# Kernel tuning notes

Measured on AMD Instinct MI355X. Metric: run time of the kernel, lower is better.

The kernel has to match this reference:

```python
import jax, jax.numpy as jnp
import numpy as np

N_FEAT = 1024
N_LAYER = 4  # n_layer + 1 in the original module


def setup_inputs() -> dict:
    key = jax.random.key(0)
    kx, kw, kb = jax.random.split(key, 3)
    x = jax.random.normal(kx, (16384, N_FEAT), dtype=jnp.float32)
    weight_w = jax.random.normal(kw, (N_LAYER, N_FEAT), dtype=jnp.float32)
    weight_b = jax.random.normal(kb, (N_LAYER, N_FEAT), dtype=jnp.float32)
    return {"x": x, "weight_w": weight_w, "weight_b": weight_b}


def reference(x, weight_w, weight_b):
    # Original per layer: x_{i+1} = x0 @ x_i^T @ w_i + b_i + x_i  (per sample).
    # (x0 x_i^T) w = x0 * <x_i, w>, so we use the O(n) equivalent form and
    # never materialize the [B, n, n] outer product.
    x0 = x  # [B, n]
    xi = x0
    for i in range(N_LAYER):
        xiw = jnp.einsum("bn,n->b", xi, weight_w[i])  # [B]
        xi = x0 * xiw[:, None] + weight_b[i][None, :] + xi
    return xi
```

## Files before the change

kernel.cpp:

```cpp
#include <hip/hip_runtime.h>

#define N_FEAT 1024
#define N_LAYER 4
#define R 2

__global__ __launch_bounds__(256, 4) void crossnet_kernel(
    const float* __restrict__ x,
    const float* __restrict__ weight_w,
    const float* __restrict__ weight_b,
    float* __restrict__ out,
    int n_rows) {
  const int wave = threadIdx.x >> 6;
  const int lane = threadIdx.x & 63;
  const int row0 = (blockIdx.x * 4 + wave) * R;
  if (row0 >= n_rows) return;

  const float4* xq = (const float4*)x;
  float4* oq = (float4*)out;

  float4 x0[R * 4];
#pragma unroll
  for (int r = 0; r < R; ++r)
#pragma unroll
    for (int c = 0; c < 4; ++c)
      x0[r * 4 + c] = xq[(size_t)(row0 + r) * 256 + c * 64 + lane];

  float p[R * N_LAYER];
#pragma unroll
  for (int k = 0; k < R * N_LAYER; ++k) p[k] = 0.f;
  float e[N_LAYER] = {0.f, 0.f, 0.f, 0.f};

#pragma unroll
  for (int c = 0; c < 4; ++c) {
    float4 w[N_LAYER];
#pragma unroll
    for (int i = 0; i < N_LAYER; ++i)
      w[i] = ((const float4*)(weight_w + i * N_FEAT))[c * 64 + lane];

    float4 cum = make_float4(0.f, 0.f, 0.f, 0.f);
#pragma unroll
    for (int i = 0; i < N_LAYER; ++i) {
      if (i > 0)
        e[i] += cum.x * w[i].x + cum.y * w[i].y + cum.z * w[i].z + cum.w * w[i].w;
      float4 b = ((const float4*)(weight_b + i * N_FEAT))[c * 64 + lane];
      cum.x += b.x; cum.y += b.y; cum.z += b.z; cum.w += b.w;
    }

#pragma unroll
    for (int r = 0; r < R; ++r) {
      const float4 xv = x0[r * 4 + c];
#pragma unroll
      for (int i = 0; i < N_LAYER; ++i) {
        p[r * N_LAYER + i] += xv.x * w[i].x + xv.y * w[i].y +
                              xv.z * w[i].z + xv.w * w[i].w;
      }
    }
  }

#pragma unroll
  for (int off = 32; off > 0; off >>= 1) {
#pragma unroll
    for (int k = 0; k < R * N_LAYER; ++k) p[k] += __shfl_xor(p[k], off, 64);
#pragma unroll
    for (int i = 1; i < N_LAYER; ++i) e[i] += __shfl_xor(e[i], off, 64);
  }

  float A[R];
#pragma unroll
  for (int r = 0; r < R; ++r) {
    A[r] = 1.f;
#pragma unroll
    for (int i = 0; i < N_LAYER; ++i)
      A[r] += A[r] * p[r * N_LAYER + i] + e[i];
  }

#pragma unroll
  for (int c = 0; c < 4; ++c) {
    float4 cum = make_float4(0.f, 0.f, 0.f, 0.f);
#pragma unroll
    for (int i = 0; i < N_LAYER; ++i) {
      float4 b = ((const float4*)(weight_b + i * N_FEAT))[c * 64 + lane];
      cum.x += b.x; cum.y += b.y; cum.z += b.z; cum.w += b.w;
    }
#pragma unroll
    for (int r = 0; r < R; ++r) {
      const float4 xv = x0[r * 4 + c];
      float4 o;
      o.x = fmaf(xv.x, A[r], cum.x);
      o.y = fmaf(xv.y, A[r], cum.y);
      o.z = fmaf(xv.z, A[r], cum.z);
      o.w = fmaf(xv.w, A[r], cum.w);
      oq[(size_t)(row0 + r) * 256 + c * 64 + lane] = o;
    }
  }
}

extern "C" void kernel_launch(void* const* d_in, const int* in_sizes, int n_in,
                              void* d_out, int out_size, void* d_ws, size_t ws_size,
                              hipStream_t stream) {
  const float* x = (const float*)d_in[0];
  const float* ww = (const float*)d_in[1];
  const float* wb = (const float*)d_in[2];
  float* out = (float*)d_out;

  int n_rows = in_sizes[0] / N_FEAT;
  int rows_per_block = 4 * R;
  int n_blocks = (n_rows + rows_per_block - 1) / rows_per_block;
  crossnet_kernel<<<n_blocks, 256, 0, stream>>>(x, ww, wb, out, n_rows);
}
```

Before: 136.3 us.

## Split row columns across wave pairs and combine partial dots via shared memory

Each block now handles 16 rows with two waves per 8-row group, each wave covering half the columns; partial dot products are exchanged through shared memory after a block barrier. x is reloaded in the output phase instead of being held in registers, and bias cumulative sums are kept from the first pass. This aims to cut register pressure and raise loads in flight, at the cost of a __syncthreads and a second read of x that relies on cache hits.

```diff
diff --git a/kernel.cpp b/kernel.cpp
--- a/kernel.cpp
+++ b/kernel.cpp
@@ -2,7 +2,7 @@
 
 #define N_FEAT 1024
 #define N_LAYER 4
-#define R 2
+#define R 8
 
 __global__ __launch_bounds__(256, 4) void crossnet_kernel(
     const float* __restrict__ x,
@@ -12,47 +12,50 @@
     int n_rows) {
   const int wave = threadIdx.x >> 6;
   const int lane = threadIdx.x & 63;
-  const int row0 = (blockIdx.x * 4 + wave) * R;
+  const int rowgrp = wave >> 1;
+  const int half = wave & 1;
+  const int row0 = blockIdx.x * (2 * R) + rowgrp * R;
   if (row0 >= n_rows) return;
 
   const float4* xq = (const float4*)x;
   float4* oq = (float4*)out;
 
-  float4 x0[R * 4];
-#pragma unroll
-  for (int r = 0; r < R; ++r)
-#pragma unroll
-    for (int c = 0; c < 4; ++c)
-      x0[r * 4 + c] = xq[(size_t)(row0 + r) * 256 + c * 64 + lane];
-
   float p[R * N_LAYER];
 #pragma unroll
   for (int k = 0; k < R * N_LAYER; ++k) p[k] = 0.f;
   float e[N_LAYER] = {0.f, 0.f, 0.f, 0.f};
+  float4 csum[2];
 
 #pragma unroll
-  for (int c = 0; c < 4; ++c) {
+  for (int lc = 0; lc < 2; ++lc) {
+    const int col = (half * 2 + lc) * 64 + lane;
+
+    float4 xv[R];
+#pragma unroll
+    for (int r = 0; r < R; ++r)
+      xv[r] = xq[(size_t)(row0 + r) * 256 + col];
+
     float4 w[N_LAYER];
 #pragma unroll
     for (int i = 0; i < N_LAYER; ++i)
-      w[i] = ((const float4*)(weight_w + i * N_FEAT))[c * 64 + lane];
+      w[i] = ((const float4*)(weight_w + i * N_FEAT))[col];
 
     float4 cum = make_float4(0.f, 0.f, 0.f, 0.f);
 #pragma unroll
     for (int i = 0; i < N_LAYER; ++i) {
       if (i > 0)
         e[i] += cum.x * w[i].x + cum.y * w[i].y + cum.z * w[i].z + cum.w * w[i].w;
-      float4 b = ((const float4*)(weight_b + i * N_FEAT))[c * 64 + lane];
+      const float4 b = ((const float4*)(weight_b + i * N_FEAT))[col];
       cum.x += b.x; cum.y += b.y; cum.z += b.z; cum.w += b.w;
     }
+    csum[lc] = cum;
 
 #pragma unroll
     for (int r = 0; r < R; ++r) {
-      const float4 xv = x0[r * 4 + c];
 #pragma unroll
       for (int i = 0; i < N_LAYER; ++i) {
-        p[r * N_LAYER + i] += xv.x * w[i].x + xv.y * w[i].y +
-                              xv.z * w[i].z + xv.w * w[i].w;
+        p[r * N_LAYER + i] += xv[r].x * w[i].x + xv[r].y * w[i].y +
+                              xv[r].z * w[i].z + xv[r].w * w[i].w;
       }
     }
   }
@@ -65,32 +68,49 @@
     for (int i = 1; i < N_LAYER; ++i) e[i] += __shfl_xor(e[i], off, 64);
   }
 
+  __shared__ float pe[4][36];
+  if (lane == 0) {
+#pragma unroll
+    for (int k = 0; k < R * N_LAYER; ++k) pe[wave][k] = p[k];
+#pragma unroll
+    for (int i = 1; i < N_LAYER; ++i) pe[wave][32 + i] = e[i];
+  }
+  __syncthreads();
+  const int partner = wave ^ 1;
+  float pp[R * N_LAYER], ep[N_LAYER];
+#pragma unroll
+  for (int k = 0; k < R * N_LAYER; ++k) pp[k] = pe[partner][k];
+  ep[0] = 0.f;
+#pragma unroll
+  for (int i = 1; i < N_LAYER; ++i) ep[i] = pe[partner][32 + i];
+
   float A[R];
 #pragma unroll
   for (int r = 0; r < R; ++r) {
     A[r] = 1.f;
 #pragma unroll
-    for (int i = 0; i < N_LAYER; ++i)
-      A[r] += A[r] * p[r * N_LAYER + i] + e[i];
+    for (int i = 0; i < N_LAYER; ++i) {
+      const float pt = p[r * N_LAYER + i] + pp[r * N_LAYER + i];
+      const float et = e[i] + ep[i];
+      A[r] += A[r] * pt + et;
+    }
   }
 
 #pragma unroll
-  for (int c = 0; c < 4; ++c) {
-    float4 cum = make_float4(0.f, 0.f, 0.f, 0.f);
+  for (int lc = 0; lc < 2; ++lc) {
+    const int col = (half * 2 + lc) * 64 + lane;
+    float4 xv[R];
 #pragma unroll
-    for (int i = 0; i < N_LAYER; ++i) {
-      float4 b = ((const float4*)(weight_b + i * N_FEAT))[c * 64 + lane];
-      cum.x += b.x; cum.y += b.y; cum.z += b.z; cum.w += b.w;
-    }
+    for (int r = 0; r < R; ++r)
+      xv[r] = xq[(size_t)(row0 + r) * 256 + col];
 #pragma unroll
     for (int r = 0; r < R; ++r) {
-      const float4 xv = x0[r * 4 + c];
       float4 o;
-      o.x = fmaf(xv.x, A[r], cum.x);
-      o.y = fmaf(xv.y, A[r], cum.y);
-      o.z = fmaf(xv.z, A[r], cum.z);
-      o.w = fmaf(xv.w, A[r], cum.w);
-      oq[(size_t)(row0 + r) * 256 + c * 64 + lane] = o;
+      o.x = fmaf(xv[r].x, A[r], csum[lc].x);
+      o.y = fmaf(xv[r].y, A[r], csum[lc].y);
+      o.z = fmaf(xv[r].z, A[r], csum[lc].z);
+      o.w = fmaf(xv[r].w, A[r], csum[lc].w);
+      oq[(size_t)(row0 + r) * 256 + col] = o;
     }
   }
 }
@@ -103,8 +123,8 @@
   const float* wb = (const float*)d_in[2];
   float* out = (float*)d_out;
 
-  int n_rows = in_sizes[0] / N_FEAT;
-  int rows_per_block = 4 * R;
-  int n_blocks = (n_rows + rows_per_block - 1) / rows_per_block;
+  const int n_rows = in_sizes[0] / N_FEAT;
+  const int rows_per_block = 2 * R;
+  const int n_blocks = (n_rows + rows_per_block - 1) / rows_per_block;
   crossnet_kernel<<<n_blocks, 256, 0, stream>>>(x, ww, wb, out, n_rows);
 }
```

Result: faster. 128.6 us (-5.6%).

## Process four rows per wave with next-pair prefetch and LDS-staged weights

Applied to the files above, without the earlier changes.

Each wave now handles four rows as two pairs. The next pair's x is loaded while the current pair's dot products and outputs are computed. Weight vectors and the cumulative bias sum are staged once per wave in shared memory, and the layer-constant e terms are reduced once, so the global weight and bias reloads per row pair go away. This halves the block count and amortizes per-wave setup. In exchange, register pressure rises from holding two pairs of rows, which could lower occupancy.

```diff
diff --git a/kernel.cpp b/kernel.cpp
--- a/kernel.cpp
+++ b/kernel.cpp
@@ -2,7 +2,8 @@
 
 #define N_FEAT 1024
 #define N_LAYER 4
-#define R 2
+#define ROWS_PER_WAVE 4
+#define PAIR 2
 
 __global__ __launch_bounds__(256, 4) void crossnet_kernel(
     const float* __restrict__ x,
@@ -12,85 +13,110 @@
     int n_rows) {
   const int wave = threadIdx.x >> 6;
   const int lane = threadIdx.x & 63;
-  const int row0 = (blockIdx.x * 4 + wave) * R;
-  if (row0 >= n_rows) return;
+
+  __shared__ float4 w_lds[N_LAYER * 256];
+  __shared__ float4 csum_lds[256];
+
+  float e[N_LAYER] = {0.f, 0.f, 0.f, 0.f};
+#pragma unroll
+  for (int c = 0; c < 4; ++c) {
+    const int col = c * 64 + lane;
+    float4 wv[N_LAYER];
+#pragma unroll
+    for (int i = 0; i < N_LAYER; ++i) {
+      wv[i] = ((const float4*)(weight_w + i * N_FEAT))[col];
+      w_lds[i * 256 + col] = wv[i];
+    }
+    float4 cum = make_float4(0.f, 0.f, 0.f, 0.f);
+#pragma unroll
+    for (int i = 0; i < N_LAYER; ++i) {
+      if (i > 0)
+        e[i] += cum.x * wv[i].x + cum.y * wv[i].y +
+                cum.z * wv[i].z + cum.w * wv[i].w;
+      const float4 b = ((const float4*)(weight_b + i * N_FEAT))[col];
+      cum.x += b.x; cum.y += b.y; cum.z += b.z; cum.w += b.w;
+    }
+    csum_lds[col] = cum;
+  }
+#pragma unroll
+  for (int off = 32; off > 0; off >>= 1)
+#pragma unroll
+    for (int i = 1; i < N_LAYER; ++i) e[i] += __shfl_xor(e[i], off, 64);
+
+  const int g = blockIdx.x * 4 + wave;
+  const int row_base = g * ROWS_PER_WAVE;
+  if (row_base >= n_rows) return;
 
   const float4* xq = (const float4*)x;
   float4* oq = (float4*)out;
 
-  float4 x0[R * 4];
+  float4 xv[PAIR][4];
 #pragma unroll
-  for (int r = 0; r < R; ++r)
+  for (int r = 0; r < PAIR; ++r)
 #pragma unroll
     for (int c = 0; c < 4; ++c)
-      x0[r * 4 + c] = xq[(size_t)(row0 + r) * 256 + c * 64 + lane];
-
-  float p[R * N_LAYER];
-#pragma unroll
-  for (int k = 0; k < R * N_LAYER; ++k) p[k] = 0.f;
-  float e[N_LAYER] = {0.f, 0.f, 0.f, 0.f};
+      xv[r][c] = xq[(size_t)(row_base + r) * 256 + c * 64 + lane];
 
 #pragma unroll
-  for (int c = 0; c < 4; ++c) {
-    float4 w[N_LAYER];
+  for (int t = 0; t < ROWS_PER_WAVE / PAIR; ++t) {
+    const int pr = row_base + t * PAIR;
+
+    float4 nxt[PAIR][4];
+    if (t + 1 < ROWS_PER_WAVE / PAIR) {
 #pragma unroll
-    for (int i = 0; i < N_LAYER; ++i)
-      w[i] = ((const float4*)(weight_w + i * N_FEAT))[c * 64 + lane];
+      for (int r = 0; r < PAIR; ++r)
+#pragma unroll
+        for (int c = 0; c < 4; ++c)
+          nxt[r][c] = xq[(size_t)(pr + PAIR + r) * 256 + c * 64 + lane];
+    }
 
-    float4 cum = make_float4(0.f, 0.f, 0.f, 0.f);
+    float p[PAIR * N_LAYER];
 #pragma unroll
-    for (int i = 0; i < N_LAYER; ++i) {
-      if (i > 0)
-        e[i] += cum.x * w[i].x + cum.y * w[i].y + cum.z * w[i].z + cum.w * w[i].w;
-      float4 b = ((const float4*)(weight_b + i * N_FEAT))[c * 64 + lane];
-      cum.x += b.x; cum.y += b.y; cum.z += b.z; cum.w += b.w;
+    for (int k = 0; k < PAIR * N_LAYER; ++k) p[k] = 0.f;
+#pragma unroll
+    for (int c = 0; c < 4; ++c) {
+      const int col = c * 64 + lane;
+#pragma unroll
+      for (int i = 0; i < N_LAYER; ++i) {
+        const float4 wv = w_lds[i * 256 + col];
+#pragma unroll
+        for (int r = 0; r < PAIR; ++r) {
+          p[r * N_LAYER + i] += xv[r][c].x * wv.x + xv[r][c].y * wv.y +
+                                xv[r][c].z * wv.z + xv[r][c].w * wv.w;
+        }
+      }
     }
 
 #pragma unroll
-    for (int r = 0; r < R; ++r) {
-      const float4 xv = x0[r * 4 + c];
+    for (int off = 32; off > 0; off >>= 1)
 #pragma unroll
-      for (int i = 0; i < N_LAYER; ++i) {
-        p[r * N_LAYER + i] += xv.x * w[i].x + xv.y * w[i].y +
-                              xv.z * w[i].z + xv.w * w[i].w;
+      for (int k = 0; k < PAIR * N_LAYER; ++k) p[k] += __shfl_xor(p[k], off, 64);
+
+#pragma unroll
+    for (int r = 0; r < PAIR; ++r) {
+      float A = 1.f;
+#pragma unroll
+      for (int i = 0; i < N_LAYER; ++i)
+        A += A * p[r * N_LAYER + i] + e[i];
+#pragma unroll
+      for (int c = 0; c < 4; ++c) {
+        const int col = c * 64 + lane;
+        const float4 cs = csum_lds[col];
+        float4 o;
+        o.x = fmaf(xv[r][c].x, A, cs.x);
+        o.y = fmaf(xv[r][c].y, A, cs.y);
+        o.z = fmaf(xv[r][c].z, A, cs.z);
+        o.w = fmaf(xv[r][c].w, A, cs.w);
+        oq[(size_t)(pr + r) * 256 + col] = o;
       }
     }
-  }
 
+    if (t + 1 < ROWS_PER_WAVE / PAIR) {
 #pragma unroll
-  for (int off = 32; off > 0; off >>= 1) {
+      for (int r = 0; r < PAIR; ++r)
 #pragma unroll
-    for (int k = 0; k < R * N_LAYER; ++k) p[k] += __shfl_xor(p[k], off, 64);
-#pragma unroll
-    for (int i = 1; i < N_LAYER; ++i) e[i] += __shfl_xor(e[i], off, 64);
-  }
-
-  float A[R];
-#pragma unroll
-  for (int r = 0; r < R; ++r) {
-    A[r] = 1.f;
-#pragma unroll
-    for (int i = 0; i < N_LAYER; ++i)
-      A[r] += A[r] * p[r * N_LAYER + i] + e[i];
-  }
-
-#pragma unroll
-  for (int c = 0; c < 4; ++c) {
-    float4 cum = make_float4(0.f, 0.f, 0.f, 0.f);
-#pragma unroll
-    for (int i = 0; i < N_LAYER; ++i) {
-      float4 b = ((const float4*)(weight_b + i * N_FEAT))[c * 64 + lane];
-      cum.x += b.x; cum.y += b.y; cum.z += b.z; cum.w += b.w;
-    }
-#pragma unroll
-    for (int r = 0; r < R; ++r) {
-      const float4 xv = x0[r * 4 + c];
-      float4 o;
-      o.x = fmaf(xv.x, A[r], cum.x);
-      o.y = fmaf(xv.y, A[r], cum.y);
-      o.z = fmaf(xv.z, A[r], cum.z);
-      o.w = fmaf(xv.w, A[r], cum.w);
-      oq[(size_t)(row0 + r) * 256 + c * 64 + lane] = o;
+        for (int c = 0; c < 4; ++c)
+          xv[r][c] = nxt[r][c];
     }
   }
 }
@@ -103,8 +129,8 @@
   const float* wb = (const float*)d_in[2];
   float* out = (float*)d_out;
 
-  int n_rows = in_sizes[0] / N_FEAT;
-  int rows_per_block = 4 * R;
-  int n_blocks = (n_rows + rows_per_block - 1) / rows_per_block;
+  const int n_rows = in_sizes[0] / N_FEAT;
+  const int rows_per_block = 4 * ROWS_PER_WAVE;
+  const int n_blocks = (n_rows + rows_per_block - 1) / rows_per_block;
   crossnet_kernel<<<n_blocks, 256, 0, stream>>>(x, ww, wb, out, n_rows);
 }
```

After: 162.7 us. 19.4% more time.
